# Kernel tuning notes

Measured on AMD Instinct MI355X. Metric: run time of the kernel, lower is better.

## Reference

```python
import jax, jax.numpy as jnp
import numpy as np

B, S, D, H = 4, 2048, 2048, 16
DH = D // H  # 128
BASE = 10000.0


def _rope_tables(seq_len, d_head, dtype):
    # inv_freq over even indices of half-dim, freqs duplicated (cat(freqs, freqs))
    inv_freq = 1.0 / (BASE ** (jnp.arange(0, d_head, 2, dtype=jnp.float32) / d_head))
    t = jnp.arange(seq_len, dtype=jnp.float32)
    freqs = jnp.einsum('i,j->ij', t, inv_freq)          # [S, d_head/2]
    emb = jnp.concatenate([freqs, freqs], axis=-1)       # [S, d_head]
    return jnp.cos(emb).astype(dtype), jnp.sin(emb).astype(dtype)


def _rotate_half(x):
    x1, x2 = jnp.split(x, 2, axis=-1)
    return jnp.concatenate([-x2, x1], axis=-1)


def setup_inputs() -> dict:
    key = jax.random.key(0)
    k1, k2, k3 = jax.random.split(key, 3)
    x = jax.random.normal(k1, (B, S, D), dtype=jnp.float32)
    Wqkv = jax.random.normal(k2, (3 * D, D), dtype=jnp.float32) * (D ** -0.5)
    Wo = jax.random.normal(k3, (D, D), dtype=jnp.float32) * (D ** -0.5)
    return {"x": x, "Wqkv": Wqkv, "Wo": Wo}


def reference(x, Wqkv, Wo) -> jnp.ndarray:
    b, s, d = x.shape
    # fused QKV projection: Linear(d, 3d, bias=False) -> x @ Wqkv.T
    qkv = jnp.einsum('bsd,ed->bse', x, Wqkv)                      # [B,S,3D]
    qkv = qkv.reshape(b, s, 3, H, DH)                              # (n n_head d_head)
    q = jnp.transpose(qkv[:, :, 0], (0, 2, 1, 3))                  # [B,H,S,DH]
    k = jnp.transpose(qkv[:, :, 1], (0, 2, 1, 3))
    v = jnp.transpose(qkv[:, :, 2], (0, 2, 1, 3))
    # rotary position embedding
    cos, sin = _rope_tables(s, DH, x.dtype)                        # [S,DH]
    cos = cos[None, None, :, :]
    sin = sin[None, None, :, :]
    q = q * cos + _rotate_half(q) * sin
    k = k * cos + _rotate_half(k) * sin
    # eval-path manual causal attention
    scale = 1.0 / jnp.sqrt(jnp.asarray(DH, dtype=x.dtype))
    scores = jnp.einsum('bhqd,bhkd->bhqk', q, k) * scale           # [B,H,S,S]
    causal = jnp.tril(jnp.ones((s, s), dtype=bool))
    scores = jnp.where(causal[None, None, :, :], scores, -jnp.inf)
    pattern = jax.nn.softmax(scores, axis=-1)
    z = jnp.einsum('bhqk,bhkd->bhqd', pattern, v)                  # [B,H,S,DH]
    z = jnp.transpose(z, (0, 2, 1, 3)).reshape(b, s, d)            # [B,S,D]
    return jnp.einsum('bsd,ed->bse', z, Wo)
```

## Files before the change

kernel.cpp:

```cpp
#include <hip/hip_runtime.h>
#include <hip/hip_bf16.h>
#include <stdint.h>

#define B_ 4
#define S_ 2048
#define D_ 2048
#define H_ 16
#define DH_ 128

typedef short bf8_t __attribute__((ext_vector_type(8)));
typedef float f4_t  __attribute__((ext_vector_type(4)));

__device__ __forceinline__ unsigned short f2bf(float f) {
  __hip_bfloat16 h = __float2bfloat16(f);
  return *reinterpret_cast<const unsigned short*>(&h);
}
__device__ __forceinline__ float bf2f(unsigned short u) {
  return __uint_as_float(((unsigned int)u) << 16);
}

__device__ __forceinline__ void gload_lds16(const void* g, void* lds) {
  __builtin_amdgcn_global_load_lds(
      (const __attribute__((address_space(1))) unsigned int*)(uintptr_t)g,
      (__attribute__((address_space(3))) unsigned int*)(unsigned int)(uintptr_t)lds,
      16, 0, 0);
}

__global__ __launch_bounds__(256) void conv_all(
    const float* __restrict__ x, const float* __restrict__ wqkv,
    const float* __restrict__ wo, unsigned short* __restrict__ xb,
    unsigned short* __restrict__ wqkvb, unsigned short* __restrict__ wob) {
  const int NX = 4194304, NQ = 3145728;
  const int TOT = 8388608, STR = 2048 * 256;
  for (int idx = blockIdx.x * 256 + threadIdx.x; idx < TOT; idx += STR) {
    const float* in;
    unsigned short* out;
    int i;
    if (idx < NX)           { in = x;    out = xb;    i = idx; }
    else if (idx < NX + NQ) { in = wqkv; out = wqkvb; i = idx - NX; }
    else                    { in = wo;   out = wob;   i = idx - NX - NQ; }
    float4 v = ((const float4*)in)[i];
    ushort4 u;
    u.x = f2bf(v.x); u.y = f2bf(v.y); u.z = f2bf(v.z); u.w = f2bf(v.w);
    ((ushort4*)out)[i] = u;
  }
}

template <int EPI>
__global__ __launch_bounds__(512, 2) void gemm256(
    const unsigned short* __restrict__ A, const unsigned short* __restrict__ Bt,
    float* __restrict__ Cf, unsigned short* __restrict__ Cb,
    int M, int N, int K) {
  __shared__ unsigned short AB[4][2][8192];
  const int tid  = threadIdx.x;
  const int lane = tid & 63;
  const int wv   = tid >> 6;
  const int wr   = wv >> 2;
  const int wc   = wv & 3;
  const int rsel = lane & 15;
  const int g    = lane >> 4;
  const int qr0  = g * 4;

  int id  = blockIdx.y * gridDim.x + blockIdx.x;
  int cpx = (gridDim.x * gridDim.y) >> 3;
  int swz = (id & 7) * cpx + (id >> 3);
  const int bm = (swz / gridDim.x) * 256;
  const int bn = (swz % gridDim.x) * 256;

  const int NS = K >> 5;

  const int ob0 = tid * 16, ob1 = ob0 + 8192;
  const int row0 = ob0 >> 6, row1 = ob1 >> 6;
  const int g0 = ((ob0 >> 4) & 3) ^ ((row0 >> 1) & 3);
  const int g1 = ((ob1 >> 4) & 3) ^ ((row1 >> 1) & 3);
  const unsigned short* Ag0 = A + (size_t)(bm + row0) * K + g0 * 8;
  const unsigned short* Ag1 = A + (size_t)(bm + row1) * K + g1 * 8;
  const unsigned short* Bg0 = Bt + (size_t)(bn + row0) * K + g0 * 8;
  const unsigned short* Bg1 = Bt + (size_t)(bn + row1) * K + g1 * 8;

  f4_t acc[8][4];
#pragma unroll
  for (int i = 0; i < 8; ++i)
#pragma unroll
    for (int j = 0; j < 4; ++j) acc[i][j] = (f4_t){0.f, 0.f, 0.f, 0.f};

  int aoff[8], boff[4];
#pragma unroll
  for (int i = 0; i < 8; ++i) {
    int arow = wr * 128 + i * 16 + rsel;
    aoff[i] = arow * 64 + ((g * 16) ^ ((arow & 6) << 3));
  }
#pragma unroll
  for (int j = 0; j < 4; ++j) {
    int brow = wc * 64 + j * 16 + rsel;
    boff[j] = brow * 64 + ((g * 16) ^ ((brow & 6) << 3));
  }

#define STAGE(sl)                                                        \
  {                                                                      \
    int slot_ = (sl) & 3;                                                \
    int ks_   = (sl) << 5;                                               \
    gload_lds16(Ag0 + ks_, (char*)&AB[slot_][0][0] + ob0);               \
    gload_lds16(Ag1 + ks_, (char*)&AB[slot_][0][0] + ob1);               \
    gload_lds16(Bg0 + ks_, (char*)&AB[slot_][1][0] + ob0);               \
    gload_lds16(Bg1 + ks_, (char*)&AB[slot_][1][0] + ob1);               \
  }

  STAGE(0); STAGE(1); STAGE(2);

  for (int s = 0; s < NS; ++s) {
    if (s < NS - 2)       asm volatile("s_waitcnt vmcnt(8)" ::: "memory");
    else if (s == NS - 2) asm volatile("s_waitcnt vmcnt(4)" ::: "memory");
    else                  asm volatile("s_waitcnt vmcnt(0)" ::: "memory");
    __builtin_amdgcn_s_barrier();
    asm volatile("" ::: "memory");

    const char* As_ = (const char*)&AB[s & 3][0][0];
    const char* Bs_ = (const char*)&AB[s & 3][1][0];
    bf8_t af[8], bfr[4];
#pragma unroll
    for (int i = 0; i < 8; ++i) af[i] = *(const bf8_t*)(As_ + aoff[i]);
#pragma unroll
    for (int j = 0; j < 4; ++j) bfr[j] = *(const bf8_t*)(Bs_ + boff[j]);

    if (s + 3 < NS) STAGE(s + 3);

    __builtin_amdgcn_s_setprio(1);
#pragma unroll
    for (int i = 0; i < 8; ++i)
#pragma unroll
      for (int j = 0; j < 4; ++j)
        acc[i][j] = __builtin_amdgcn_mfma_f32_16x16x32_bf16(af[i], bfr[j], acc[i][j], 0, 0, 0);
    __builtin_amdgcn_s_setprio(0);
  }
#undef STAGE

#pragma unroll
  for (int i = 0; i < 8; ++i) {
#pragma unroll
    for (int j = 0; j < 4; ++j) {
#pragma unroll
      for (int r = 0; r < 4; ++r) {
        int row = bm + wr * 128 + i * 16 + qr0 + r;
        int col = bn + wc * 64 + j * 16 + rsel;
        float v = acc[i][j][r];
        if (EPI == 0) {
          Cf[(size_t)row * N + col] = v;
        } else {
          int c = col >> 11, h = (col >> 7) & (H_ - 1), dh = col & (DH_ - 1);
          int b = row >> 11, s = row & (S_ - 1);
          size_t dst = ((((size_t)c * B_ + b) * H_ + h) * S_ + s) * DH_ + dh;
          Cb[dst] = f2bf(v);
        }
      }
    }
  }
}

__global__ void rope_tab(float* __restrict__ tc, float* __restrict__ ts) {
  int s = blockIdx.x;
  int i = threadIdx.x;
  float inv = powf(10000.0f, -(float)i / 64.0f);
  float f   = (float)s * inv;
  tc[s * 64 + i] = cosf(f);
  ts[s * 64 + i] = sinf(f);
}

__global__ __launch_bounds__(256) void rope_k(
    unsigned short* __restrict__ Kk,
    const float* __restrict__ tc, const float* __restrict__ ts) {
  int idx = blockIdx.x * 256 + threadIdx.x;
  int iv  = idx & 7;
  int s   = (idx >> 3) & (S_ - 1);
  int bh  = idx >> 14;
  size_t base = ((size_t)bh * S_ + s) * DH_;
  int i0 = iv * 8;
  bf8_t x1 = *(const bf8_t*)&Kk[base + i0];
  bf8_t x2 = *(const bf8_t*)&Kk[base + i0 + 64];
  const float* tcp = tc + s * 64 + i0;
  const float* tsp = ts + s * 64 + i0;
  bf8_t y1, y2;
#pragma unroll
  for (int e = 0; e < 8; ++e) {
    float c = tcp[e], sn = tsp[e];
    float a = bf2f((unsigned short)x1[e]);
    float b = bf2f((unsigned short)x2[e]);
    y1[e] = (short)f2bf(a * c - b * sn);
    y2[e] = (short)f2bf(b * c + a * sn);
  }
  *(bf8_t*)&Kk[base + i0]      = y1;
  *(bf8_t*)&Kk[base + i0 + 64] = y2;
}

__global__ __launch_bounds__(512) void attn_fwd(
    const unsigned short* __restrict__ Q, const unsigned short* __restrict__ Kk,
    const unsigned short* __restrict__ V, unsigned short* __restrict__ Z,
    const float* __restrict__ tabc, const float* __restrict__ tabs) {
  __shared__ unsigned short Ks[3][64 * 128];
  __shared__ unsigned short Vt[2][128 * 64];
  __shared__ unsigned short Pw[8][32 * 64];
  const int tid  = threadIdx.x;
  const int lane = tid & 63;
  const int wv   = tid >> 6;

  int id  = blockIdx.y * gridDim.x + blockIdx.x;
  int x   = id & 7;
  int idx = id >> 3;
  const int bh = x * 8 + (idx & 7);
  const int q0 = (7 - (idx >> 3)) * 256;

  const size_t base = (size_t)bh * S_ * DH_;
  const int rsel = lane & 15;
  const int g    = lane >> 4;
  const int kof  = g * 8;
  const int qr0  = g * 4;
  const int qlo  = q0 + wv * 32;
  const int qhi  = qlo + 31;
  const float sl2 = 0.08838834764831845f * 1.4426950408889634f;

  bf8_t aq[2][4];
#pragma unroll
  for (int rg = 0; rg < 2; ++rg) {
    const int qrow = qlo + rg * 16 + rsel;
#pragma unroll
    for (int kc = 0; kc < 4; ++kc)
      aq[rg][kc] = *(const bf8_t*)&Q[base + (size_t)qrow * DH_ + kc * 32 + kof];
    const float* tcr = tabc + (size_t)qrow * 64;
    const float* tsr = tabs + (size_t)qrow * 64;
#pragma unroll
    for (int kc = 0; kc < 2; ++kc)
#pragma unroll
      for (int e = 0; e < 8; ++e) {
        int i = kc * 32 + kof + e;
        float c  = tcr[i], sn = tsr[i];
        float x1 = bf2f((unsigned short)aq[rg][kc][e]);
        float x2 = bf2f((unsigned short)aq[rg][kc + 2][e]);
        aq[rg][kc][e]     = (short)f2bf((x1 * c - x2 * sn) * sl2);
        aq[rg][kc + 2][e] = (short)f2bf((x2 * c + x1 * sn) * sl2);
      }
  }

  bf8_t vones;
#pragma unroll
  for (int e = 0; e < 8; ++e) vones[e] = (short)0x3F80;

  f4_t o[2][9];
#pragma unroll
  for (int rg = 0; rg < 2; ++rg)
#pragma unroll
    for (int nf = 0; nf < 9; ++nf) o[rg][nf] = (f4_t){0.f, 0.f, 0.f, 0.f};
  float mrow[2][4] = {{-3e30f, -3e30f, -3e30f, -3e30f},
                      {-3e30f, -3e30f, -3e30f, -3e30f}};
  const int nt = q0 / 64 + 4;

  const int kvp = tid & 31;
  const int vc0 = (tid >> 5) * 8;

#define KSTAGE(tt)                                                            \
  {                                                                           \
    const unsigned short* gK_ = Kk + base + (size_t)(tt) * 64 * DH_;          \
    int slot_ = (tt) % 3;                                                     \
    _Pragma("unroll")                                                         \
    for (int c = 0; c < 2; ++c) {                                             \
      int ob = (c * 512 + tid) * 16;                                          \
      int row = ob >> 8;                                                      \
      int scol = (ob & 255) ^ ((row & 7) << 4);                               \
      gload_lds16(gK_ + (size_t)row * DH_ + (scol >> 1),                      \
                  (char*)&Ks[slot_][0] + ob);                                 \
    }                                                                         \
  }
#define VTWRITE(buf_)                                                         \
  {                                                                           \
    unsigned int* Vt32 = (unsigned int*)&Vt[buf_][0];                         \
    _Pragma("unroll")                                                         \
    for (int e = 0; e < 8; ++e) {                                             \
      unsigned int val = (unsigned short)vlo[e] |                             \
                         ((unsigned int)(unsigned short)vhi[e] << 16);        \
      Vt32[(vc0 + e) * 32 + (kvp ^ (e << 2))] = val;                          \
    }                                                                         \
  }

  bf8_t vlo, vhi;
  vlo = *(const bf8_t*)&V[base + (size_t)(2 * kvp) * DH_ + vc0];
  vhi = *(const bf8_t*)&V[base + (size_t)(2 * kvp + 1) * DH_ + vc0];
  KSTAGE(0);
  KSTAGE(1);
  VTWRITE(0);

  for (int t = 0; t < nt; ++t) {
    const int curV = t & 1;
    const int curK = t % 3;
    const bool pfV = (t + 1 < nt);
    const bool pfK = (t + 2 < nt);

    if (pfV) asm volatile("s_waitcnt vmcnt(2)" ::: "memory");
    else     asm volatile("s_waitcnt vmcnt(0)" ::: "memory");
    asm volatile("s_waitcnt lgkmcnt(0)" ::: "memory");
    __builtin_amdgcn_s_barrier();
    asm volatile("" ::: "memory");

    if (pfV) {
      const unsigned short* gV = V + base + (size_t)(t + 1) * 64 * DH_;
      vlo = *(const bf8_t*)&gV[(size_t)(2 * kvp) * DH_ + vc0];
      vhi = *(const bf8_t*)&gV[(size_t)(2 * kvp + 1) * DH_ + vc0];
    }
    if (pfK) KSTAGE(t + 2);

    const int kv0 = t * 64;
    const bool active = (kv0 <= qhi);
    const bool domask = active && (kv0 + 63 > qlo);

    if (active) {
      f4_t sacc[2][4];
#pragma unroll
      for (int rg = 0; rg < 2; ++rg)
#pragma unroll
        for (int cf = 0; cf < 4; ++cf) sacc[rg][cf] = (f4_t){0.f, 0.f, 0.f, 0.f};
      __builtin_amdgcn_s_setprio(1);
#pragma unroll
      for (int cf = 0; cf < 4; ++cf)
#pragma unroll
        for (int kc = 0; kc < 4; ++kc) {
          int krow = cf * 16 + rsel;
          bf8_t bk = *(const bf8_t*)&Ks[curK][krow * 128 + ((kc * 32 + kof) ^ ((krow & 7) << 3))];
          sacc[0][cf] = __builtin_amdgcn_mfma_f32_16x16x32_bf16(aq[0][kc], bk, sacc[0][cf], 0, 0, 0);
          sacc[1][cf] = __builtin_amdgcn_mfma_f32_16x16x32_bf16(aq[1][kc], bk, sacc[1][cf], 0, 0, 0);
        }
      __builtin_amdgcn_s_setprio(0);

      if (domask) {
#pragma unroll
        for (int rg = 0; rg < 2; ++rg)
#pragma unroll
          for (int cf = 0; cf < 4; ++cf) {
            int kvabs = kv0 + cf * 16 + rsel;
#pragma unroll
            for (int r = 0; r < 4; ++r) {
              int qabs = qlo + rg * 16 + qr0 + r;
              if (kvabs > qabs) sacc[rg][cf][r] = -3e30f;
            }
          }
      }

      float tmr[2][4];
      bool needr = false;
#pragma unroll
      for (int rg = 0; rg < 2; ++rg)
#pragma unroll
        for (int r = 0; r < 4; ++r) {
          tmr[rg][r] = fmaxf(fmaxf(sacc[rg][0][r], sacc[rg][1][r]),
                             fmaxf(sacc[rg][2][r], sacc[rg][3][r]));
          needr = needr || (tmr[rg][r] > mrow[rg][r] + 11.f);
        }
      if (__any(needr)) {
#pragma unroll
        for (int rg = 0; rg < 2; ++rg)
#pragma unroll
          for (int r = 0; r < 4; ++r) {
            float m = tmr[rg][r];
#pragma unroll
            for (int d = 1; d < 16; d <<= 1) m = fmaxf(m, __shfl_xor(m, d, 16));
            float nm = fmaxf(mrow[rg][r], m);
            float sc = exp2f(mrow[rg][r] - nm);
            mrow[rg][r] = nm;
#pragma unroll
            for (int nf = 0; nf < 9; ++nf) o[rg][nf][r] *= sc;
          }
      }
#pragma unroll
      for (int rg = 0; rg < 2; ++rg)
#pragma unroll
        for (int cf = 0; cf < 4; ++cf)
#pragma unroll
          for (int r = 0; r < 4; ++r)
            sacc[rg][cf][r] = exp2f(sacc[rg][cf][r] - mrow[rg][r]);

      unsigned short* P = &Pw[wv][0];
#pragma unroll
      for (int rg = 0; rg < 2; ++rg)
#pragma unroll
        for (int cf = 0; cf < 4; ++cf)
#pragma unroll
          for (int r = 0; r < 4; ++r) {
            int prow = rg * 16 + qr0 + r;
            P[prow * 64 + ((cf * 16 + rsel) ^ (((prow >> 1) & 7) << 3))] = f2bf(sacc[rg][cf][r]);
          }
    }

    if (pfV) VTWRITE(curV ^ 1);

    if (active) {
      unsigned short* P = &Pw[wv][0];
      __builtin_amdgcn_s_setprio(1);
#pragma unroll
      for (int kc2 = 0; kc2 < 2; ++kc2) {
        bf8_t pa0, pa1;
        {
          int pr0 = rsel;
          int pr1 = 16 + rsel;
          pa0 = *(const bf8_t*)&P[pr0 * 64 + ((kc2 * 32 + kof) ^ (((pr0 >> 1) & 7) << 3))];
          pa1 = *(const bf8_t*)&P[pr1 * 64 + ((kc2 * 32 + kof) ^ (((pr1 >> 1) & 7) << 3))];
        }
#pragma unroll
        for (int nf = 0; nf < 8; ++nf) {
          int vrow = nf * 16 + rsel;
          bf8_t bv = *(const bf8_t*)&Vt[curV][vrow * 64 + ((kc2 * 32 + kof) ^ ((vrow & 7) << 3))];
          o[0][nf] = __builtin_amdgcn_mfma_f32_16x16x32_bf16(pa0, bv, o[0][nf], 0, 0, 0);
          o[1][nf] = __builtin_amdgcn_mfma_f32_16x16x32_bf16(pa1, bv, o[1][nf], 0, 0, 0);
        }
        o[0][8] = __builtin_amdgcn_mfma_f32_16x16x32_bf16(pa0, vones, o[0][8], 0, 0, 0);
        o[1][8] = __builtin_amdgcn_mfma_f32_16x16x32_bf16(pa1, vones, o[1][8], 0, 0, 0);
      }
      __builtin_amdgcn_s_setprio(0);
    }
  }
#undef KSTAGE
#undef VTWRITE

  const int b = bh >> 4, h = bh & 15;
#pragma unroll
  for (int rg = 0; rg < 2; ++rg)
#pragma unroll
    for (int r = 0; r < 4; ++r) {
      float inv = 1.0f / o[rg][8][r];
      int s = qlo + rg * 16 + qr0 + r;
      size_t rowo = ((size_t)b * S_ + s) * D_ + h * DH_;
#pragma unroll
      for (int nf = 0; nf < 8; ++nf)
        Z[rowo + nf * 16 + rsel] = f2bf(o[rg][nf][r] * inv);
    }
}

extern "C" void kernel_launch(void* const* d_in, const int* in_sizes, int n_in,
                              void* d_out, int out_size, void* d_ws, size_t ws_size,
                              hipStream_t stream) {
  const float* x    = (const float*)d_in[0];
  const float* Wqkv = (const float*)d_in[1];
  const float* Wo   = (const float*)d_in[2];
  float* out = (float*)d_out;

  const size_t QKV_ELEMS = (size_t)B_ * H_ * S_ * DH_;
  char* w = (char*)d_ws;
  unsigned short* xb = (unsigned short*)w;
  unsigned short* z  = xb;
  w += (size_t)8192 * 2048 * 2;
  unsigned short* wqkvb = (unsigned short*)w; w += (size_t)6144 * 2048 * 2;
  unsigned short* wob   = (unsigned short*)w; w += (size_t)2048 * 2048 * 2;
  unsigned short* qq = (unsigned short*)w;    w += QKV_ELEMS * 2;
  unsigned short* kk = (unsigned short*)w;    w += QKV_ELEMS * 2;
  unsigned short* vv = (unsigned short*)w;    w += QKV_ELEMS * 2;
  float* tabc = (float*)w; w += (size_t)S_ * 64 * 4;
  float* tabs = (float*)w; w += (size_t)S_ * 64 * 4;
  if ((size_t)(w - (char*)d_ws) > ws_size) return;

  conv_all<<<2048, 256, 0, stream>>>(x, Wqkv, Wo, xb, wqkvb, wob);
  gemm256<1><<<dim3(24, 32), 512, 0, stream>>>(xb, wqkvb, nullptr, qq, 8192, 6144, 2048);
  rope_tab<<<2048, 64, 0, stream>>>(tabc, tabs);
  rope_k<<<4096, 256, 0, stream>>>(kk, tabc, tabs);
  attn_fwd<<<dim3(S_ / 256, B_ * H_), 512, 0, stream>>>(qq, kk, vv, z, tabc, tabs);
  gemm256<0><<<dim3(8, 32), 512, 0, stream>>>(z, wob, out, nullptr, 8192, 2048, 2048);
}
```

Before: 415.7 us.

## Use eight-phase ping-pong pipelined GEMM for QKV projection

Adds a new GEMM kernel, used only for the QKV projection, that stages 64-wide K tiles in double-buffered LDS split by half-tile. It interleaves global-to-LDS loads for the next tile with eight barrier-separated MFMA phases per iteration, and uses an 8-way XOR swizzle for 128-byte rows. The aim is to overlap memory traffic with compute in finer steps and reduce LDS bank conflicts. In exchange it adds many more barriers per K step and carries some risk that the vmcnt accounting is wrong. The output projection keeps the old kernel.

```diff
diff --git a/kernel.cpp b/kernel.cpp
--- a/kernel.cpp
+++ b/kernel.cpp
@@ -47,11 +47,11 @@
 }
 
 template <int EPI>
-__global__ __launch_bounds__(512, 2) void gemm256(
+__global__ __launch_bounds__(512, 2) void gemm8p(
     const unsigned short* __restrict__ A, const unsigned short* __restrict__ Bt,
     float* __restrict__ Cf, unsigned short* __restrict__ Cb,
     int M, int N, int K) {
-  __shared__ unsigned short AB[4][2][8192];
+  __shared__ unsigned short LDSm[2][2][2][8192];
   const int tid  = threadIdx.x;
   const int lane = tid & 63;
   const int wv   = tid >> 6;
@@ -67,16 +67,11 @@
   const int bm = (swz / gridDim.x) * 256;
   const int bn = (swz % gridDim.x) * 256;
 
-  const int NS = K >> 5;
-
-  const int ob0 = tid * 16, ob1 = ob0 + 8192;
-  const int row0 = ob0 >> 6, row1 = ob1 >> 6;
-  const int g0 = ((ob0 >> 4) & 3) ^ ((row0 >> 1) & 3);
-  const int g1 = ((ob1 >> 4) & 3) ^ ((row1 >> 1) & 3);
-  const unsigned short* Ag0 = A + (size_t)(bm + row0) * K + g0 * 8;
-  const unsigned short* Ag1 = A + (size_t)(bm + row1) * K + g1 * 8;
-  const unsigned short* Bg0 = Bt + (size_t)(bn + row0) * K + g0 * 8;
-  const unsigned short* Bg1 = Bt + (size_t)(bn + row1) * K + g1 * 8;
+  const int NT = K >> 6;
+  const int NI = NT >> 1;
+
+  const int sz0 = ((g) ^ (rsel & 7)) << 4;
+  const int sz1 = ((4 + g) ^ (rsel & 7)) << 4;
 
   f4_t acc[8][4];
 #pragma unroll
@@ -84,56 +79,94 @@
 #pragma unroll
     for (int j = 0; j < 4; ++j) acc[i][j] = (f4_t){0.f, 0.f, 0.f, 0.f};
 
-  int aoff[8], boff[4];
-#pragma unroll
-  for (int i = 0; i < 8; ++i) {
-    int arow = wr * 128 + i * 16 + rsel;
-    aoff[i] = arow * 64 + ((g * 16) ^ ((arow & 6) << 3));
-  }
-#pragma unroll
-  for (int j = 0; j < 4; ++j) {
-    int brow = wc * 64 + j * 16 + rsel;
-    boff[j] = brow * 64 + ((g * 16) ^ ((brow & 6) << 3));
-  }
-
-#define STAGE(sl)                                                        \
-  {                                                                      \
-    int slot_ = (sl) & 3;                                                \
-    int ks_   = (sl) << 5;                                               \
-    gload_lds16(Ag0 + ks_, (char*)&AB[slot_][0][0] + ob0);               \
-    gload_lds16(Ag1 + ks_, (char*)&AB[slot_][0][0] + ob1);               \
-    gload_lds16(Bg0 + ks_, (char*)&AB[slot_][1][0] + ob0);               \
-    gload_lds16(Bg1 + ks_, (char*)&AB[slot_][1][0] + ob1);               \
-  }
-
-  STAGE(0); STAGE(1); STAGE(2);
-
-  for (int s = 0; s < NS; ++s) {
-    if (s < NS - 2)       asm volatile("s_waitcnt vmcnt(8)" ::: "memory");
-    else if (s == NS - 2) asm volatile("s_waitcnt vmcnt(4)" ::: "memory");
-    else                  asm volatile("s_waitcnt vmcnt(0)" ::: "memory");
-    __builtin_amdgcn_s_barrier();
-    asm volatile("" ::: "memory");
-
-    const char* As_ = (const char*)&AB[s & 3][0][0];
-    const char* Bs_ = (const char*)&AB[s & 3][1][0];
-    bf8_t af[8], bfr[4];
-#pragma unroll
-    for (int i = 0; i < 8; ++i) af[i] = *(const bf8_t*)(As_ + aoff[i]);
-#pragma unroll
-    for (int j = 0; j < 4; ++j) bfr[j] = *(const bf8_t*)(Bs_ + boff[j]);
-
-    if (s + 3 < NS) STAGE(s + 3);
-
-    __builtin_amdgcn_s_setprio(1);
-#pragma unroll
-    for (int i = 0; i < 8; ++i)
-#pragma unroll
-      for (int j = 0; j < 4; ++j)
-        acc[i][j] = __builtin_amdgcn_mfma_f32_16x16x32_bf16(af[i], bfr[j], acc[i][j], 0, 0, 0);
-    __builtin_amdgcn_s_setprio(0);
-  }
-#undef STAGE
+  bf8_t af[2][2];
+  bf8_t bfr[4][2];
+
+#define STG(m_, h_, X_)                                                       \
+  {                                                                           \
+    const unsigned short* P_ = (m_ == 0) ? A : Bt;                            \
+    int rb_ = (m_ == 0) ? bm : bn;                                            \
+    _Pragma("unroll")                                                         \
+    for (int u_ = 0; u_ < 2; ++u_) {                                          \
+      int ob_  = (u_ * 512 + tid) * 16;                                       \
+      int row_ = ob_ >> 7;                                                    \
+      int G_   = ((ob_ >> 4) & 7) ^ (row_ & 7);                               \
+      gload_lds16(P_ + (size_t)(rb_ + (h_) * 128 + row_) * K + (X_) * 64 + G_ * 8, \
+                  (char*)&LDSm[(X_) & 1][m_][h_][0] + ob_);                   \
+    }                                                                         \
+  }
+#define RD_A(bu_, q_)                                                         \
+  {                                                                           \
+    const char* Ab_ = (const char*)&LDSm[bu_][0][wr][0];                      \
+    af[0][0] = *(const bf8_t*)(Ab_ + ((q_) * 32 + rsel) * 128 + sz0);         \
+    af[0][1] = *(const bf8_t*)(Ab_ + ((q_) * 32 + rsel) * 128 + sz1);         \
+    af[1][0] = *(const bf8_t*)(Ab_ + ((q_) * 32 + 16 + rsel) * 128 + sz0);    \
+    af[1][1] = *(const bf8_t*)(Ab_ + ((q_) * 32 + 16 + rsel) * 128 + sz1);    \
+  }
+#define RD_B(bu_)                                                             \
+  {                                                                           \
+    const char* Bb_ = (const char*)&LDSm[bu_][1][wc >> 1][0];                 \
+    _Pragma("unroll")                                                         \
+    for (int j_ = 0; j_ < 4; ++j_) {                                          \
+      int rlb_ = (wc & 1) * 64 + j_ * 16 + rsel;                              \
+      bfr[j_][0] = *(const bf8_t*)(Bb_ + rlb_ * 128 + sz0);                   \
+      bfr[j_][1] = *(const bf8_t*)(Bb_ + rlb_ * 128 + sz1);                   \
+    }                                                                         \
+  }
+#define MM(q_)                                                                \
+  __builtin_amdgcn_s_setprio(1);                                              \
+  _Pragma("unroll")                                                           \
+  for (int i2_ = 0; i2_ < 2; ++i2_)                                           \
+    _Pragma("unroll")                                                         \
+    for (int j_ = 0; j_ < 4; ++j_) {                                          \
+      acc[(q_) * 2 + i2_][j_] = __builtin_amdgcn_mfma_f32_16x16x32_bf16(      \
+          af[i2_][0], bfr[j_][0], acc[(q_) * 2 + i2_][j_], 0, 0, 0);          \
+      acc[(q_) * 2 + i2_][j_] = __builtin_amdgcn_mfma_f32_16x16x32_bf16(      \
+          af[i2_][1], bfr[j_][1], acc[(q_) * 2 + i2_][j_], 0, 0, 0);          \
+    }                                                                         \
+  __builtin_amdgcn_s_setprio(0);
+#define BAR() { __builtin_amdgcn_s_barrier(); asm volatile("" ::: "memory"); }
+
+  STG(1, 0, 0); STG(1, 1, 0); STG(0, 0, 0); STG(0, 1, 0);
+  STG(1, 0, 1); STG(1, 1, 1);
+  asm volatile("s_waitcnt vmcnt(4)" ::: "memory");
+  BAR();
+
+  for (int it = 0; it < NI; ++it) {
+    const int T = it * 2;
+    const bool c2 = (T + 2 < NT);
+
+    RD_A(0, 0); RD_B(0);
+    STG(0, 0, T + 1);
+    BAR(); MM(0); BAR();
+    RD_A(0, 1);
+    STG(0, 1, T + 1);
+    BAR(); MM(1); BAR();
+    RD_A(0, 2);
+    if (c2) STG(1, 0, T + 2);
+    BAR(); MM(2); BAR();
+    RD_A(0, 3);
+    if (c2) { STG(1, 1, T + 2); asm volatile("s_waitcnt vmcnt(4)" ::: "memory"); }
+    else    { asm volatile("s_waitcnt vmcnt(0)" ::: "memory"); }
+    BAR(); MM(3); BAR();
+    RD_A(1, 0); RD_B(1);
+    if (c2) STG(0, 0, T + 2);
+    BAR(); MM(0); BAR();
+    RD_A(1, 1);
+    if (c2) STG(0, 1, T + 2);
+    BAR(); MM(1); BAR();
+    RD_A(1, 2);
+    if (c2) STG(1, 0, T + 3);
+    BAR(); MM(2); BAR();
+    RD_A(1, 3);
+    if (c2) { STG(1, 1, T + 3); asm volatile("s_waitcnt vmcnt(4)" ::: "memory"); }
+    BAR(); MM(3); BAR();
+  }
+#undef STG
+#undef RD_A
+#undef RD_B
+#undef MM
+#undef BAR
 
 #pragma unroll
   for (int i = 0; i < 8; ++i) {
@@ -157,6 +190,117 @@
   }
 }
 
+template <int EPI>
+__global__ __launch_bounds__(512, 2) void gemm256(
+    const unsigned short* __restrict__ A, const unsigned short* __restrict__ Bt,
+    float* __restrict__ Cf, unsigned short* __restrict__ Cb,
+    int M, int N, int K) {
+  __shared__ unsigned short AB[4][2][8192];
+  const int tid  = threadIdx.x;
+  const int lane = tid & 63;
+  const int wv   = tid >> 6;
+  const int wr   = wv >> 2;
+  const int wc   = wv & 3;
+  const int rsel = lane & 15;
+  const int g    = lane >> 4;
+  const int qr0  = g * 4;
+
+  int id  = blockIdx.y * gridDim.x + blockIdx.x;
+  int cpx = (gridDim.x * gridDim.y) >> 3;
+  int swz = (id & 7) * cpx + (id >> 3);
+  const int bm = (swz / gridDim.x) * 256;
+  const int bn = (swz % gridDim.x) * 256;
+
+  const int NS = K >> 5;
+
+  const int ob0 = tid * 16, ob1 = ob0 + 8192;
+  const int row0 = ob0 >> 6, row1 = ob1 >> 6;
+  const int g0 = ((ob0 >> 4) & 3) ^ ((row0 >> 1) & 3);
+  const int g1 = ((ob1 >> 4) & 3) ^ ((row1 >> 1) & 3);
+  const unsigned short* Ag0 = A + (size_t)(bm + row0) * K + g0 * 8;
+  const unsigned short* Ag1 = A + (size_t)(bm + row1) * K + g1 * 8;
+  const unsigned short* Bg0 = Bt + (size_t)(bn + row0) * K + g0 * 8;
+  const unsigned short* Bg1 = Bt + (size_t)(bn + row1) * K + g1 * 8;
+
+  f4_t acc[8][4];
+#pragma unroll
+  for (int i = 0; i < 8; ++i)
+#pragma unroll
+    for (int j = 0; j < 4; ++j) acc[i][j] = (f4_t){0.f, 0.f, 0.f, 0.f};
+
+  int aoff[8], boff[4];
+#pragma unroll
+  for (int i = 0; i < 8; ++i) {
+    int arow = wr * 128 + i * 16 + rsel;
+    aoff[i] = arow * 64 + ((g * 16) ^ ((arow & 6) << 3));
+  }
+#pragma unroll
+  for (int j = 0; j < 4; ++j) {
+    int brow = wc * 64 + j * 16 + rsel;
+    boff[j] = brow * 64 + ((g * 16) ^ ((brow & 6) << 3));
+  }
+
+#define STAGE(sl)                                                        \
+  {                                                                      \
+    int slot_ = (sl) & 3;                                                \
+    int ks_   = (sl) << 5;                                               \
+    gload_lds16(Ag0 + ks_, (char*)&AB[slot_][0][0] + ob0);               \
+    gload_lds16(Ag1 + ks_, (char*)&AB[slot_][0][0] + ob1);               \
+    gload_lds16(Bg0 + ks_, (char*)&AB[slot_][1][0] + ob0);               \
+    gload_lds16(Bg1 + ks_, (char*)&AB[slot_][1][0] + ob1);               \
+  }
+
+  STAGE(0); STAGE(1); STAGE(2);
+
+  for (int s = 0; s < NS; ++s) {
+    if (s < NS - 2)       asm volatile("s_waitcnt vmcnt(8)" ::: "memory");
+    else if (s == NS - 2) asm volatile("s_waitcnt vmcnt(4)" ::: "memory");
+    else                  asm volatile("s_waitcnt vmcnt(0)" ::: "memory");
+    __builtin_amdgcn_s_barrier();
+    asm volatile("" ::: "memory");
+
+    const char* As_ = (const char*)&AB[s & 3][0][0];
+    const char* Bs_ = (const char*)&AB[s & 3][1][0];
+    bf8_t af[8], bfr[4];
+#pragma unroll
+    for (int i = 0; i < 8; ++i) af[i] = *(const bf8_t*)(As_ + aoff[i]);
+#pragma unroll
+    for (int j = 0; j < 4; ++j) bfr[j] = *(const bf8_t*)(Bs_ + boff[j]);
+
+    if (s + 3 < NS) STAGE(s + 3);
+
+    __builtin_amdgcn_s_setprio(1);
+#pragma unroll
+    for (int i = 0; i < 8; ++i)
+#pragma unroll
+      for (int j = 0; j < 4; ++j)
+        acc[i][j] = __builtin_amdgcn_mfma_f32_16x16x32_bf16(af[i], bfr[j], acc[i][j], 0, 0, 0);
+    __builtin_amdgcn_s_setprio(0);
+  }
+#undef STAGE
+
+#pragma unroll
+  for (int i = 0; i < 8; ++i) {
+#pragma unroll
+    for (int j = 0; j < 4; ++j) {
+#pragma unroll
+      for (int r = 0; r < 4; ++r) {
+        int row = bm + wr * 128 + i * 16 + qr0 + r;
+        int col = bn + wc * 64 + j * 16 + rsel;
+        float v = acc[i][j][r];
+        if (EPI == 0) {
+          Cf[(size_t)row * N + col] = v;
+        } else {
+          int c = col >> 11, h = (col >> 7) & (H_ - 1), dh = col & (DH_ - 1);
+          int b = row >> 11, s = row & (S_ - 1);
+          size_t dst = ((((size_t)c * B_ + b) * H_ + h) * S_ + s) * DH_ + dh;
+          Cb[dst] = f2bf(v);
+        }
+      }
+    }
+  }
+}
+
 __global__ void rope_tab(float* __restrict__ tc, float* __restrict__ ts) {
   int s = blockIdx.x;
   int i = threadIdx.x;
@@ -454,7 +598,7 @@
   if ((size_t)(w - (char*)d_ws) > ws_size) return;
 
   conv_all<<<2048, 256, 0, stream>>>(x, Wqkv, Wo, xb, wqkvb, wob);
-  gemm256<1><<<dim3(24, 32), 512, 0, stream>>>(xb, wqkvb, nullptr, qq, 8192, 6144, 2048);
+  gemm8p<1><<<dim3(24, 32), 512, 0, stream>>>(xb, wqkvb, nullptr, qq, 8192, 6144, 2048);
   rope_tab<<<2048, 64, 0, stream>>>(tabc, tabs);
   rope_k<<<4096, 256, 0, stream>>>(kk, tabc, tabs);
   attn_fwd<<<dim3(S_ / 256, B_ * H_), 512, 0, stream>>>(qq, kk, vv, z, tabc, tabs);
```

After: 407.8 us (median of 3 runs). About the same (-1.9%).
